# Kernel tuning notes

Hardware: AMD Instinct MI355X
Metric: run time of the kernel (lower is better)

Reference implementation:

```python
import jax, jax.numpy as jnp
import numpy as np

B, N = 4, 8192


def setup_inputs() -> dict:
    key = jax.random.key(0)
    k1, k2, k3 = jax.random.split(key, 3)
    pc_pred = jax.random.normal(k1, (B, N, 3), dtype=jnp.float32)
    pc_target = jax.random.normal(k2, (B, N, 3), dtype=jnp.float32)
    fbpp = jax.random.uniform(k3, (B,), dtype=jnp.float32)
    return {"pc_pred": pc_pred, "pc_target": pc_target, "fbpp": fbpp, "lam": 1}


def _chamfer(x, y):
    # x: (B, N, 3), y: (B, M, 3)
    x2 = jnp.sum(x * x, axis=-1)                     # (B, N)
    y2 = jnp.sum(y * y, axis=-1)                     # (B, M)
    xy = jnp.einsum('bnd,bmd->bnm', x, y)            # (B, N, M)
    d2 = jnp.maximum(x2[:, :, None] + y2[:, None, :] - 2.0 * xy, 0.0)
    cham_x = jnp.mean(jnp.min(d2, axis=2), axis=1)   # (B,) pred -> target
    cham_y = jnp.mean(jnp.min(d2, axis=1), axis=1)   # (B,) target -> pred
    return jnp.mean(cham_x + cham_y)                 # scalar (batch mean)


def reference(pc_pred, pc_target, fbpp, lam):
    d = _chamfer(pc_pred, pc_target)
    r = jnp.mean(fbpp)
    return d + lam * r
```

## Files before the change

kernel.cpp:

```cpp
#include <hip/hip_runtime.h>
#include <math.h>


typedef __attribute__((ext_vector_type(8)))  short  short8;
typedef __attribute__((ext_vector_type(16))) float  f32x16;

#define YS      4
#define RPB     256
#define YTILE_T 32

#define MFMA2(da, db, A, B0, B1) \
    asm("v_mfma_f32_32x32x16_bf16 %0, %2, %3, 0\n\t" \
        "v_mfma_f32_32x32x16_bf16 %1, %2, %4, 0\n\t" \
        "s_nop 7\n\t" \
        "s_nop 7" \
        : "=&v"(da), "=&v"(db) \
        : "v"(A), "v"(B0), "v"(B1))

static inline int roundup_h(int v, int a) { return (v + a - 1) / a * a; }

static __device__ __forceinline__ unsigned short f2bf(float f) {
    union { float f; unsigned int u; } v; v.f = f;
    unsigned int r = v.u + 0x7FFFu + ((v.u >> 16) & 1u);
    return (unsigned short)(r >> 16);
}
static __device__ __forceinline__ float bf2f(unsigned short s) {
    union { unsigned int u; float f; } v; v.u = ((unsigned int)s) << 16;
    return v.f;
}
static __device__ __forceinline__ unsigned int pk2(unsigned short lo,
                                                   unsigned short hi) {
    return (unsigned int)lo | ((unsigned int)hi << 16);
}

static __device__ __forceinline__ float allmin32(float v) {
    union { float f; int i; } u, t;
    u.f = v;
    t.i = __builtin_amdgcn_update_dpp(u.i, u.i, 0xB1, 0xF, 0xF, false);
    u.f = fminf(u.f, t.f);
    t.i = __builtin_amdgcn_update_dpp(u.i, u.i, 0x4E, 0xF, 0xF, false);
    u.f = fminf(u.f, t.f);
    t.i = __builtin_amdgcn_update_dpp(u.i, u.i, 0x124, 0xF, 0xF, false);
    u.f = fminf(u.f, t.f);
    t.i = __builtin_amdgcn_update_dpp(u.i, u.i, 0x128, 0xF, 0xF, false);
    u.f = fminf(u.f, t.f);
    t.i = __builtin_amdgcn_ds_swizzle(u.i, 0x401F);
    u.f = fminf(u.f, t.f);
    return u.f;
}

__global__ __launch_bounds__(256) void pack_kernel(
    const float* __restrict__ pred, const float* __restrict__ targ,
    int B, int N, int M, int NpadP, int NpadT,
    unsigned short* __restrict__ aP, unsigned short* __restrict__ bP,
    unsigned short* __restrict__ aT, unsigned short* __restrict__ bT)
{
    const int padmax = (NpadP > NpadT) ? NpadP : NpadT;
    const int gid = blockIdx.x * 256 + threadIdx.x;
    if (gid >= B * padmax) return;
    const int b = gid / padmax, i = gid - b * padmax;

    for (int cloud = 0; cloud < 2; ++cloud) {
        const int cnt  = cloud ? M : N;
        const int npad = cloud ? NpadT : NpadP;
        if (i >= npad) continue;
        const float* src = (cloud ? targ : pred) +
                           ((size_t)b * cnt + min(i, cnt - 1)) * 3;
        unsigned short* A  = (cloud ? aT : aP) + ((size_t)b * npad + i) * 16;
        unsigned short* Bk = (cloud ? bT : bP) + (size_t)b * npad * 16;

        const float xs[3] = {src[0], src[1], src[2]};
        const float n2 = xs[0]*xs[0] + xs[1]*xs[1] + xs[2]*xs[2];
        unsigned short th[3], tl[3], yh[3], yl[3];
        #pragma unroll
        for (int c = 0; c < 3; ++c) {
            const float t = -2.0f * xs[c];
            th[c] = f2bf(t);     tl[c] = f2bf(t - bf2f(th[c]));
            yh[c] = f2bf(xs[c]); yl[c] = f2bf(xs[c] - bf2f(yh[c]));
        }
        const unsigned short n2h = f2bf(n2);
        const unsigned short n2l = f2bf(n2 - bf2f(n2h));
        const unsigned short ONE = 0x3F80;

        uint4 alo, ahi, blo, bhi;
        alo.x = pk2(th[0], th[1]); alo.y = pk2(th[2], tl[0]);
        alo.z = pk2(tl[1], tl[2]); alo.w = pk2(th[0], th[1]);
        ahi.x = pk2(th[2], tl[0]); ahi.y = pk2(tl[1], tl[2]);
        ahi.z = pk2(ONE,  ONE);    ahi.w = pk2(n2h,  n2l);
        blo.x = pk2(yh[0], yh[1]); blo.y = pk2(yh[2], yh[0]);
        blo.z = pk2(yh[1], yh[2]); blo.w = pk2(yl[0], yl[1]);
        bhi.x = pk2(yl[2], yl[0]); bhi.y = pk2(yl[1], yl[2]);
        bhi.z = pk2(n2h,  n2l);    bhi.w = pk2(ONE,  ONE);

        *(uint4*)(A)     = alo;  *(uint4*)(A + 8) = ahi;
        const size_t tb = (size_t)(i >> 5) * 64 + (i & 31);
        *(uint4*)(Bk + tb * 8)        = blo;
        *(uint4*)(Bk + (tb + 32) * 8) = bhi;
    }
}

__global__ __launch_bounds__(256, 4) void mfma_sweep(
    const unsigned short* __restrict__ aP, const unsigned short* __restrict__ bP,
    const unsigned short* __restrict__ aT, const unsigned short* __restrict__ bT,
    int B, int N, int M, int NpadP, int NpadT, int NpadMax,
    float* __restrict__ rowpart)
{
    const int tid  = threadIdx.x;
    const int w    = tid >> 6;
    const int lane = tid & 63;
    const int lc   = lane & 31, h = lane >> 5;

    const int SP = NpadMax / RPB;
    int t = blockIdx.x;
    const int sp  = t % SP;  t /= SP;
    const int js  = t % YS;  t /= YS;
    const int b   = t % B;   t /= B;
    const int dir = t;

    const unsigned short* Xp = (dir == 0) ? aP : aT;
    const unsigned short* Yp = (dir == 0) ? bT : bP;
    const int NpadX = (dir == 0) ? NpadP : NpadT;
    const int NpadY = (dir == 0) ? NpadT : NpadP;
    const int Nx    = (dir == 0) ? N : M;
    if (sp * RPB >= NpadX) return;

    const int TM  = NpadY / 32;
    const int nt0 = (TM + YS - 1) / YS;
    const int t0  = js * nt0;
    const int nt  = min(TM - t0, nt0);
    if (nt <= 0) return;

    __shared__ unsigned short ypack[YTILE_T * 32 * 16];

    const int row0 = sp * RPB + w * 64;
    const size_t abase = ((size_t)b * NpadX + row0 + lc) * 16 + (size_t)h * 8;
    const short8 a0 = *reinterpret_cast<const short8*>(Xp + abase);
    const short8 a1 = *reinterpret_cast<const short8*>(Xp + abase + 32 * 16);

    f32x16 rm0, rm1;
    #pragma unroll
    for (int r = 0; r < 16; ++r) {
        rm0[r] = __builtin_inff(); rm1[r] = __builtin_inff();
    }

    for (int f0 = 0; f0 < nt; f0 += YTILE_T) {
        const int fc = min(YTILE_T, nt - f0);
        __syncthreads();
        {
            const unsigned short* src =
                Yp + ((size_t)b * NpadY + (size_t)(t0 + f0) * 32) * 16;
            const int units = fc * 64;
            for (int u = tid; u < units; u += 256)
                *(uint4*)&ypack[(size_t)u * 8] =
                    *(const uint4*)(src + (size_t)u * 8);
        }
        __syncthreads();

        for (int j = 0; j < fc; j += 2) {
            const short8 bq0 = *reinterpret_cast<const short8*>(
                &ypack[(size_t)j * 512 + (size_t)lane * 8]);
            const short8 bq1 = (j + 1 < fc)
                ? *reinterpret_cast<const short8*>(
                      &ypack[(size_t)(j + 1) * 512 + (size_t)lane * 8])
                : bq0;
            {
                f32x16 da, db;
                MFMA2(da, db, a0, bq0, bq1);
                #pragma unroll
                for (int r = 0; r < 16; ++r)
                    rm0[r] = fminf(fminf(da[r], db[r]), rm0[r]);
            }
            {
                f32x16 da, db;
                MFMA2(da, db, a1, bq0, bq1);
                #pragma unroll
                for (int r = 0; r < 16; ++r)
                    rm1[r] = fminf(fminf(da[r], db[r]), rm1[r]);
            }
        }
    }

    const size_t outb = (((size_t)dir * B + b) * YS + js) * (size_t)NpadMax;
    #pragma unroll
    for (int r = 0; r < 16; ++r) {
        const float v0 = allmin32(rm0[r]);
        const float v1 = allmin32(rm1[r]);
        if (lc == 0) {
            const int rr = (r & 3) + 8 * (r >> 2) + 4 * h;
            const int ra = row0 + rr, rb = row0 + 32 + rr;
            if (ra < Nx) rowpart[outb + ra] = v0;
            if (rb < Nx) rowpart[outb + rb] = v1;
        }
    }
}

__global__ __launch_bounds__(256) void combine_kernel(
    const float* __restrict__ rowpart, int B, int N, int M,
    int NpadP, int NpadT, int NpadMax,
    float invBN, float invBM, float* __restrict__ partial)
{
    const int tid = threadIdx.x;
    const int tot = 2 * B * NpadMax;
    float acc = 0.f;
    for (int idx = blockIdx.x * 256 + tid; idx < tot; idx += gridDim.x * 256) {
        const int row = idx % NpadMax;
        const int rem = idx / NpadMax;
        const int b   = rem % B;
        const int dir = rem / B;
        const int Nx  = (dir == 0) ? N : M;
        if (row >= Nx) continue;
        const int NpadY = (dir == 0) ? NpadT : NpadP;
        const int TM  = NpadY / 32;
        const int nt0 = (TM + YS - 1) / YS;
        float m = __builtin_inff();
        #pragma unroll
        for (int js = 0; js < YS; ++js)
            if (js * nt0 < TM)
                m = fminf(m, rowpart[(((size_t)dir * B + b) * YS + js)
                                     * (size_t)NpadMax + row]);
        acc += fmaxf(m, 0.f) * ((dir == 0) ? invBN : invBM);
    }
    __shared__ float sb[256];
    sb[tid] = acc; __syncthreads();
    for (int off2 = 128; off2 > 0; off2 >>= 1) {
        if (tid < off2) sb[tid] += sb[tid + off2];
        __syncthreads();
    }
    if (tid == 0) partial[blockIdx.x] = sb[0];
}

__global__ void finalize_kernel(const float* __restrict__ partial, int np,
                                const float* __restrict__ fbpp, int Bf,
                                const void* __restrict__ lamp,
                                float* __restrict__ out)
{
    __shared__ float sb[256];
    const int tid = threadIdx.x;
    float acc = 0.f;
    for (int i = tid; i < np; i += 256) acc += partial[i];
    sb[tid] = acc;
    __syncthreads();
    for (int off = 128; off > 0; off >>= 1) {
        if (tid < off) sb[tid] += sb[tid + off];
        __syncthreads();
    }
    if (tid == 0) {
        const int li = *(const int*)lamp;
        const float lam = (li >= -1000000 && li <= 1000000)
                            ? (float)li : *(const float*)lamp;
        float fm = 0.f;
        for (int i = 0; i < Bf; ++i) fm += fbpp[i];
        fm /= (float)Bf;
        out[0] = sb[0] + lam * fm;
    }
}

extern "C" void kernel_launch(void* const* d_in, const int* in_sizes, int n_in,
                              void* d_out, int out_size, void* d_ws, size_t ws_size,
                              hipStream_t stream) {
    const float* pred = (const float*)d_in[0];
    const float* targ = (const float*)d_in[1];
    const float* fbpp = (const float*)d_in[2];
    const void*  lamp = d_in[3];

    const int B = in_sizes[2];
    const int N = in_sizes[0] / (3 * B);
    const int M = in_sizes[1] / (3 * B);
    const int NpadP = roundup_h(N, RPB);
    const int NpadT = roundup_h(M, RPB);
    const int NpadMax = (NpadP > NpadT) ? NpadP : NpadT;

    size_t o = 0;
    auto take = [&](size_t bytes) {
        size_t r = o; o += (bytes + 255) & ~(size_t)255; return r;
    };
    unsigned short* aP = (unsigned short*)((char*)d_ws +
                         take(((size_t)B * NpadP + 64) * 32));
    unsigned short* bP = (unsigned short*)((char*)d_ws +
                         take(((size_t)B * NpadP + 64) * 32));
    unsigned short* aT = (unsigned short*)((char*)d_ws +
                         take(((size_t)B * NpadT + 64) * 32));
    unsigned short* bT = (unsigned short*)((char*)d_ws +
                         take(((size_t)B * NpadT + 64) * 32));
    float* rowpart = (float*)((char*)d_ws +
                     take((size_t)2 * B * YS * NpadMax * sizeof(float)));
    float* partial = (float*)((char*)d_ws + take(256 * sizeof(float)));
    (void)ws_size;

    pack_kernel<<<(B * NpadMax + 255) / 256, 256, 0, stream>>>(
        pred, targ, B, N, M, NpadP, NpadT, aP, bP, aT, bT);

    const int SP = NpadMax / RPB;
    const int blocks = 2 * B * YS * SP;
    mfma_sweep<<<blocks, 256, 0, stream>>>(
        aP, bP, aT, bT, B, N, M, NpadP, NpadT, NpadMax, rowpart);

    combine_kernel<<<256, 256, 0, stream>>>(
        rowpart, B, N, M, NpadP, NpadT, NpadMax,
        1.f / ((float)B * (float)N), 1.f / ((float)B * (float)M), partial);

    finalize_kernel<<<1, 256, 0, stream>>>(partial, 256, fbpp, B, lamp,
                                           (float*)d_out);
}
```

Measured before the change: 39.25 us.

## Stream Y tiles directly from global memory with register prefetch instead of LDS staging

The sweep kernel no longer stages Y tiles into shared memory behind __syncthreads barriers. Each wave now loads its B operands straight from global memory, prefetching the next pair of tiles into registers while the current pair feeds the MFMAs. This removes LDS traffic and block-wide barriers but relies on L1/L2 caching of Y, since all four waves of a block read the same data. It also assumes TM divides evenly by YS and by 2, dropping the ragged-tail guards here and in combine_kernel, and it pads the workspace so the prefetch can read past the end.

```diff
diff --git a/kernel.cpp b/kernel.cpp
--- a/kernel.cpp
+++ b/kernel.cpp
@@ -7,7 +7,6 @@
 
 #define YS      4
 #define RPB     256
-#define YTILE_T 32
 
 #define MFMA2(da, db, A, B0, B1) \
     asm("v_mfma_f32_32x32x16_bf16 %0, %2, %3, 0\n\t" \
@@ -125,12 +124,8 @@
     if (sp * RPB >= NpadX) return;
 
     const int TM  = NpadY / 32;
-    const int nt0 = (TM + YS - 1) / YS;
+    const int nt0 = TM / YS;
     const int t0  = js * nt0;
-    const int nt  = min(TM - t0, nt0);
-    if (nt <= 0) return;
-
-    __shared__ unsigned short ypack[YTILE_T * 32 * 16];
 
     const int row0 = sp * RPB + w * 64;
     const size_t abase = ((size_t)b * NpadX + row0 + lc) * 16 + (size_t)h * 8;
@@ -143,41 +138,31 @@
         rm0[r] = __builtin_inff(); rm1[r] = __builtin_inff();
     }
 
-    for (int f0 = 0; f0 < nt; f0 += YTILE_T) {
-        const int fc = min(YTILE_T, nt - f0);
-        __syncthreads();
+    const unsigned short* yp =
+        Yp + (size_t)b * NpadY * 16 + (size_t)t0 * 512 + (size_t)lane * 8;
+    short8 c0 = *reinterpret_cast<const short8*>(yp);
+    short8 c1 = *reinterpret_cast<const short8*>(yp + 512);
+
+    for (int j = 0; j < nt0; j += 2) {
+        const short8 n0 = *reinterpret_cast<const short8*>(yp + 1024);
+        const short8 n1 = *reinterpret_cast<const short8*>(yp + 1536);
+        yp += 1024;
+        __builtin_amdgcn_sched_barrier(0);
         {
-            const unsigned short* src =
-                Yp + ((size_t)b * NpadY + (size_t)(t0 + f0) * 32) * 16;
-            const int units = fc * 64;
-            for (int u = tid; u < units; u += 256)
-                *(uint4*)&ypack[(size_t)u * 8] =
-                    *(const uint4*)(src + (size_t)u * 8);
-        }
-        __syncthreads();
-
-        for (int j = 0; j < fc; j += 2) {
-            const short8 bq0 = *reinterpret_cast<const short8*>(
-                &ypack[(size_t)j * 512 + (size_t)lane * 8]);
-            const short8 bq1 = (j + 1 < fc)
-                ? *reinterpret_cast<const short8*>(
-                      &ypack[(size_t)(j + 1) * 512 + (size_t)lane * 8])
-                : bq0;
-            {
-                f32x16 da, db;
-                MFMA2(da, db, a0, bq0, bq1);
-                #pragma unroll
-                for (int r = 0; r < 16; ++r)
-                    rm0[r] = fminf(fminf(da[r], db[r]), rm0[r]);
-            }
-            {
-                f32x16 da, db;
-                MFMA2(da, db, a1, bq0, bq1);
-                #pragma unroll
-                for (int r = 0; r < 16; ++r)
-                    rm1[r] = fminf(fminf(da[r], db[r]), rm1[r]);
-            }
-        }
+            f32x16 da, db;
+            MFMA2(da, db, a0, c0, c1);
+            #pragma unroll
+            for (int r = 0; r < 16; ++r)
+                rm0[r] = fminf(fminf(da[r], db[r]), rm0[r]);
+        }
+        {
+            f32x16 da, db;
+            MFMA2(da, db, a1, c0, c1);
+            #pragma unroll
+            for (int r = 0; r < 16; ++r)
+                rm1[r] = fminf(fminf(da[r], db[r]), rm1[r]);
+        }
+        c0 = n0; c1 = n1;
     }
 
     const size_t outb = (((size_t)dir * B + b) * YS + js) * (size_t)NpadMax;
@@ -209,15 +194,11 @@
         const int dir = rem / B;
         const int Nx  = (dir == 0) ? N : M;
         if (row >= Nx) continue;
-        const int NpadY = (dir == 0) ? NpadT : NpadP;
-        const int TM  = NpadY / 32;
-        const int nt0 = (TM + YS - 1) / YS;
         float m = __builtin_inff();
         #pragma unroll
         for (int js = 0; js < YS; ++js)
-            if (js * nt0 < TM)
-                m = fminf(m, rowpart[(((size_t)dir * B + b) * YS + js)
-                                     * (size_t)NpadMax + row]);
+            m = fminf(m, rowpart[(((size_t)dir * B + b) * YS + js)
+                                 * (size_t)NpadMax + row]);
         acc += fmaxf(m, 0.f) * ((dir == 0) ? invBN : invBM);
     }
     __shared__ float sb[256];
@@ -275,13 +256,13 @@
         size_t r = o; o += (bytes + 255) & ~(size_t)255; return r;
     };
     unsigned short* aP = (unsigned short*)((char*)d_ws +
-                         take(((size_t)B * NpadP + 64) * 32));
+                         take((size_t)B * NpadP * 32 + 8192));
     unsigned short* bP = (unsigned short*)((char*)d_ws +
-                         take(((size_t)B * NpadP + 64) * 32));
+                         take((size_t)B * NpadP * 32 + 8192));
     unsigned short* aT = (unsigned short*)((char*)d_ws +
-                         take(((size_t)B * NpadT + 64) * 32));
+                         take((size_t)B * NpadT * 32 + 8192));
     unsigned short* bT = (unsigned short*)((char*)d_ws +
-                         take(((size_t)B * NpadT + 64) * 32));
+                         take((size_t)B * NpadT * 32 + 8192));
     float* rowpart = (float*)((char*)d_ws +
                      take((size_t)2 * B * YS * NpadMax * sizeof(float)));
     float* partial = (float*)((char*)d_ws + take(256 * sizeof(float)));
```

Measured after the change: 38.85 us. About the same (-1.0%).
